# Optimization experiments

Hardware: AMD Instinct MI355X
Metric: run time of the kernel (lower is better)

The kernel has to match this reference:

```python
import jax, jax.numpy as jnp
import numpy as np

VOCAB, EDIM, HDIM, ODIM = 100000, 128, 128, 10
BN_EPS = 1e-3  # keras BatchNormalization default epsilon


def _bn(x, gamma, beta, axes):
    # training-mode batch norm (batch statistics), as in a Keras training step
    m = jnp.mean(x, axis=axes, keepdims=True)
    v = jnp.var(x, axis=axes, keepdims=True)
    return gamma * (x - m) * jax.lax.rsqrt(v + BN_EPS) + beta


def _lstm_last(x, mask, W, U, b):
    # Keras LSTM, gate order [i, f, c, o]; masked steps carry state through.
    # x: [B,T,E], mask: [B,T] bool. Returns final hidden state [B,H].
    B, T, _ = x.shape
    H = U.shape[0]
    xg = jnp.einsum('bte,eg->btg', x, W) + b  # precomputed input projections [B,T,4H]

    def step(carry, inp):
        h, c = carry
        g, m = inp                      # g: [B,4H], m: [B]
        g = g + h @ U
        i, f, cc, o = jnp.split(g, 4, axis=-1)
        c_new = jax.nn.sigmoid(f) * c + jax.nn.sigmoid(i) * jnp.tanh(cc)
        h_new = jax.nn.sigmoid(o) * jnp.tanh(c_new)
        m = m[:, None]
        return (jnp.where(m, h_new, h), jnp.where(m, c_new, c)), None

    init = (jnp.zeros((B, H), x.dtype), jnp.zeros((B, H), x.dtype))
    (h, _), _ = jax.lax.scan(step, init, (xg.transpose(1, 0, 2), mask.T))
    return h


def setup_inputs() -> dict:
    key = jax.random.key(0)
    ks = jax.random.split(key, 12)
    s = 0.05
    ids = jax.random.randint(ks[0], (128, 1024), 0, VOCAB)
    return {
        'ids': ids,
        'embed_table': jax.random.normal(ks[1], (VOCAB, EDIM), jnp.float32) * s,
        'gamma1': jnp.ones((EDIM,), jnp.float32),
        'beta1': jnp.zeros((EDIM,), jnp.float32),
        'Wf': jax.random.normal(ks[2], (EDIM, 4 * HDIM), jnp.float32) * s,
        'Uf': jax.random.normal(ks[3], (HDIM, 4 * HDIM), jnp.float32) * s,
        'bf': jnp.zeros((4 * HDIM,), jnp.float32),
        'Wb': jax.random.normal(ks[4], (EDIM, 4 * HDIM), jnp.float32) * s,
        'Ub': jax.random.normal(ks[5], (HDIM, 4 * HDIM), jnp.float32) * s,
        'bb': jnp.zeros((4 * HDIM,), jnp.float32),
        'gamma2': jnp.ones((2 * HDIM,), jnp.float32),
        'beta2': jnp.zeros((2 * HDIM,), jnp.float32),
        'Wd': jax.random.normal(ks[6], (2 * HDIM, ODIM), jnp.float32) * s,
        'bd': jnp.zeros((ODIM,), jnp.float32),
    }


def reference(ids, embed_table, gamma1, beta1, Wf, Uf, bf, Wb, Ub, bb,
              gamma2, beta2, Wd, bd):
    mask = ids != 0                              # mask_zero=True
    x = embed_table[ids]                         # [B,T,E]
    x = _bn(x, gamma1, beta1, axes=(0, 1))
    h_fwd = _lstm_last(x, mask, Wf, Uf, bf)      # forward direction
    h_bwd = _lstm_last(x[:, ::-1], mask[:, ::-1], Wb, Ub, bb)  # go_backwards
    h = jnp.concatenate([h_fwd, h_bwd], axis=-1)  # merge_mode='concat' -> [B,2H]
    h = _bn(h, gamma2, beta2, axes=(0,))
    return jax.nn.softmax(h @ Wd + bd, axis=-1)
```

## Files before the change

### kernel.cpp

```cpp
#include <hip/hip_runtime.h>
#include <hip/hip_bf16.h>
#include <stdint.h>

#define VOCAB  100000
#define EDIM   128
#define HDIM   128
#define T_LEN  1024
#define BATCH  128
#define GDIM   512
#define NROWS  (BATCH*T_LEN)
#define BN_EPS 1e-3f

using short8 = __attribute__((ext_vector_type(8))) short;
using f32x4  = __attribute__((ext_vector_type(4))) float;

#define WS_SCALE  0u
#define WS_SHIFT  512u
#define WS_PSUM   1024u
#define WS_PSQ    (WS_PSUM + 524288u)
#define WS_HCAT   (WS_PSQ + 524288u)
#define WS_FRAGS  (WS_HCAT + 131072u)
#define WS_XN     (WS_FRAGS + 524288u)

#define SGI_K (-1.4426950408889634f)
#define SGC_K ( 2.8853900817779268f)

__device__ __forceinline__ short f2bf(float f) {
    uint32_t u = __float_as_uint(f);
    return (short)((u + 0x7fffu + ((u >> 16) & 1u)) >> 16);
}

#define BAR() asm volatile("s_waitcnt lgkmcnt(0)\n\ts_barrier" ::: "memory")

__global__ void k_bn1_partial(const int* __restrict__ ids,
                              const float* __restrict__ tab,
                              float* __restrict__ psum, float* __restrict__ psq) {
    __shared__ float ls[256], lq[256];
    int f = threadIdx.x & 127, rr = threadIdx.x >> 7;
    int r0 = blockIdx.x * 128;
    float s = 0.f, q = 0.f;
    for (int r = rr; r < 128; r += 2) {
        int id = ids[r0 + r];
        float v = tab[(size_t)id * EDIM + f];
        s += v; q += v * v;
    }
    ls[threadIdx.x] = s; lq[threadIdx.x] = q;
    __syncthreads();
    if (threadIdx.x < 128) {
        psum[blockIdx.x * 128 + f] = ls[f] + ls[f + 128];
        psq [blockIdx.x * 128 + f] = lq[f] + lq[f + 128];
    }
}

__global__ void k_bn1_final(const float* __restrict__ psum, const float* __restrict__ psq,
                            const float* __restrict__ gamma, const float* __restrict__ beta,
                            float* __restrict__ scale, float* __restrict__ shift) {
    int f = threadIdx.x;
    float s = 0.f, q = 0.f;
    for (int p = 0; p < 1024; ++p) { s += psum[p * 128 + f]; q += psq[p * 128 + f]; }
    const float inv_n = 1.0f / (float)NROWS;
    float m  = s * inv_n;
    float v  = q * inv_n - m * m;
    float sc = gamma[f] * rsqrtf(v + BN_EPS);
    scale[f] = sc;
    shift[f] = beta[f] - m * sc;
}

__global__ void k_packmask(const int* __restrict__ ids, unsigned long long* __restrict__ mwords) {
    int gid = blockIdx.x * 1024 + threadIdx.x;
    unsigned long long bal = __ballot(ids[gid] != 0);
    if ((threadIdx.x & 63) == 0) mwords[gid >> 6] = bal;
}

__global__ void k_embed_norm(const int* __restrict__ ids,
                             const float* __restrict__ tab,
                             const float* __restrict__ scale,
                             const float* __restrict__ shift,
                             short* __restrict__ xn) {
    int gid = blockIdx.x * blockDim.x + threadIdx.x;
    int row = gid >> 4, seg = gid & 15;
    int id  = ids[row];
    const float* src = tab + (size_t)id * EDIM + seg * 8;
    short8 out;
#pragma unroll
    for (int j = 0; j < 8; ++j) {
        float v = scale[seg * 8 + j] * src[j] + shift[seg * 8 + j];
        out[j] = f2bf(v);
    }
    *(short8*)(xn + (size_t)row * EDIM + seg * 8) = out;
}

__global__ void k_prepack(const float* __restrict__ Wf, const float* __restrict__ Uf,
                          const float* __restrict__ Wb, const float* __restrict__ Ub,
                          short* __restrict__ frags) {
    int gid = blockIdx.x * blockDim.x + threadIdx.x;
    int l  = gid & 63;
    int f  = (gid >> 6) & 31;
    int w  = (gid >> 11) & 7;
    int d  = gid >> 14;
    int s    = f >> 4;
    int gate = (f >> 2) & 3;
    int kc   = f & 3;
    const float* M = s ? (d ? Ub : Uf) : (d ? Wb : Wf);
    const float gs = (gate == 2) ? SGC_K : SGI_K;
    int rbase = 32 * kc + 8 * (l >> 4);
    int col   = 128 * gate + 16 * w + (l & 15);
    short8 out;
#pragma unroll
    for (int j = 0; j < 8; ++j) out[j] = f2bf(gs * M[(size_t)(rbase + j) * GDIM + col]);
    *(short8*)(frags + (size_t)gid * 8) = out;
}

#define MFMA(A, B, C) __builtin_amdgcn_mfma_f32_16x16x32_bf16((A), (B), (C), 0, 0, 0)
#define S8(x) __builtin_bit_cast(short8, x)

__global__ void __launch_bounds__(512, 2)
k_lstm(const short* __restrict__ xn,
       const short* __restrict__ frags,
       const unsigned long long* __restrict__ mwords,
       const float* __restrict__ bf_, const float* __restrict__ bb_,
       float* __restrict__ hcat) {
    const int d   = blockIdx.x >> 7;
    const int b   = blockIdx.x & 127;
    const int tid = threadIdx.x;
    const int w   = tid >> 6, l = tid & 63, g = l >> 4, li = l & 15;

    __shared__ float xg_lds[2][16][512];
    __shared__ __align__(16) short h_s[2][HDIM];

    float* const xgf = &xg_lds[0][0][0];
    float* const xgr = xgf + (w * 16 + li) * 4;

    const short8* wsrc = (const short8*)frags + (size_t)(d * 8 + w) * 32 * 64 + l;

    short8 wq00 = wsrc[0*64],  wq01 = wsrc[1*64],  wq02 = wsrc[2*64],  wq03 = wsrc[3*64];
    short8 wq10 = wsrc[4*64],  wq11 = wsrc[5*64],  wq12 = wsrc[6*64],  wq13 = wsrc[7*64];
    short8 wq20 = wsrc[8*64],  wq21 = wsrc[9*64],  wq22 = wsrc[10*64], wq23 = wsrc[11*64];
    short8 wq30 = wsrc[12*64], wq31 = wsrc[13*64], wq32 = wsrc[14*64], wq33 = wsrc[15*64];

    short8 u00 = wsrc[(16+0)*64],  u01 = wsrc[(16+1)*64],  u02 = wsrc[(16+2)*64],  u03 = wsrc[(16+3)*64];
    short8 u10 = wsrc[(16+4)*64],  u11 = wsrc[(16+5)*64],  u12 = wsrc[(16+6)*64],  u13 = wsrc[(16+7)*64];
    short8 u20 = wsrc[(16+8)*64],  u21 = wsrc[(16+9)*64],  u22 = wsrc[(16+10)*64], u23 = wsrc[(16+11)*64];
    short8 u30 = wsrc[(16+12)*64], u31 = wsrc[(16+13)*64], u32 = wsrc[(16+14)*64], u33 = wsrc[(16+15)*64];

    const float* bias = d ? bb_ : bf_;
    const float bia0 = bias[0*128 + w*16 + li] * SGI_K;
    const float bia1 = bias[1*128 + w*16 + li] * SGI_K;
    const float bia2 = bias[2*128 + w*16 + li] * SGC_K;
    const float bia3 = bias[3*128 + w*16 + li] * SGI_K;

    if (tid < HDIM) h_s[0][tid] = 0;
    float c_reg = 0.f, h_reg = 0.f;

    const f32x4 Z = {0.f, 0.f, 0.f, 0.f};

    uint4 ga0, ga1, ga2, ga3;
#define GATHER(C_) { \
        int s0_ = 16 * (C_) + li; \
        int p_  = d ? (T_LEN - 1 - s0_) : s0_; \
        const uint4* gb_ = (const uint4*)xn + (size_t)(b * T_LEN + p_) * 16; \
        ga0 = gb_[g]; ga1 = gb_[4 + g]; ga2 = gb_[8 + g]; ga3 = gb_[12 + g]; \
    }

#define XWGATE(GG, W0, W1, W2, W3, BIA, BUF) { \
        f32x4 ax = {(BIA), (BIA), (BIA), (BIA)}; \
        ax = MFMA(S8(ga0), W0, ax); \
        ax = MFMA(S8(ga1), W1, ax); \
        ax = MFMA(S8(ga2), W2, ax); \
        ax = MFMA(S8(ga3), W3, ax); \
        float* dst_ = xgf + (BUF) * 8192 + (w * 16 + li) * 4 + (GG); \
        dst_[(4*g+0)*512] = ax[0]; dst_[(4*g+1)*512] = ax[1]; \
        dst_[(4*g+2)*512] = ax[2]; dst_[(4*g+3)*512] = ax[3]; \
    }

    GATHER(0);
    XWGATE(0, wq00, wq01, wq02, wq03, bia0, 0);
    XWGATE(1, wq10, wq11, wq12, wq13, bia1, 0);
    XWGATE(2, wq20, wq21, wq22, wq23, bia2, 0);
    XWGATE(3, wq30, wq31, wq32, wq33, bia3, 0);
    __syncthreads();

    float xa0, xa1, xa2, xa3, xb0, xb1, xb2, xb3;
    {
        const f32x4 xv0 = *(const f32x4*)(xgr);
        xa0 = xv0[0]; xa1 = xv0[1]; xa2 = xv0[2]; xa3 = xv0[3];
    }

#define STEP(J, XC0, XC1, XC2, XC3, XN0, XN1, XN2, XN3) { \
        const uint4* hp_ = (const uint4*)(h_s[(J) & 1]); \
        uint4 hf0 = hp_[g], hf1 = hp_[4 + g], hf2 = hp_[8 + g], hf3 = hp_[12 + g]; \
        if (c < 63) { \
            if ((J) == 8)  XWGATE(0, wq00, wq01, wq02, wq03, bia0, ((c + 1) & 1)); \
            if ((J) == 9)  XWGATE(1, wq10, wq11, wq12, wq13, bia1, ((c + 1) & 1)); \
            if ((J) == 10) XWGATE(2, wq20, wq21, wq22, wq23, bia2, ((c + 1) & 1)); \
            if ((J) == 11) XWGATE(3, wq30, wq31, wq32, wq33, bia3, ((c + 1) & 1)); \
        } \
        f32x4 p0 = MFMA(S8(hf0), u00, Z); \
        f32x4 p1 = MFMA(S8(hf0), u10, Z); \
        f32x4 p2 = MFMA(S8(hf0), u20, Z); \
        f32x4 p3 = MFMA(S8(hf0), u30, Z); \
        f32x4 q0 = MFMA(S8(hf2), u02, Z); \
        f32x4 q1 = MFMA(S8(hf2), u12, Z); \
        f32x4 q2 = MFMA(S8(hf2), u22, Z); \
        f32x4 q3 = MFMA(S8(hf2), u32, Z); \
        p0 = MFMA(S8(hf1), u01, p0); \
        p1 = MFMA(S8(hf1), u11, p1); \
        p2 = MFMA(S8(hf1), u21, p2); \
        p3 = MFMA(S8(hf1), u31, p3); \
        q0 = MFMA(S8(hf3), u03, q0); \
        q1 = MFMA(S8(hf3), u13, q1); \
        q2 = MFMA(S8(hf3), u23, q2); \
        q3 = MFMA(S8(hf3), u33, q3); \
        if (!((c == 63) && ((J) == 15))) { \
            const f32x4 xv_ = *(const f32x4*)(xgr + (((J) < 15) ? (c & 1) : ((c + 1) & 1)) * 8192 \
                                                  + (((J) + 1) & 15) * 512); \
            XN0 = xv_[0]; XN1 = xv_[1]; XN2 = xv_[2]; XN3 = xv_[3]; \
        } \
        { \
            float gi = (XC0) + (p0[0] + q0[0]); \
            float gf = (XC1) + (p1[0] + q1[0]); \
            float gc = (XC2) + (p2[0] + q2[0]); \
            float go = (XC3) + (p3[0] + q3[0]); \
            float si = __builtin_amdgcn_rcpf(1.f + exp2f(gi)); \
            float sf = __builtin_amdgcn_rcpf(1.f + exp2f(gf)); \
            float so = __builtin_amdgcn_rcpf(1.f + exp2f(go)); \
            float tc = __builtin_fmaf(-2.f, __builtin_amdgcn_rcpf(1.f + exp2f(gc)), 1.f); \
            float cn = __builtin_fmaf(sf, c_reg, si * tc); \
            float th = __builtin_fmaf(-2.f, __builtin_amdgcn_rcpf(1.f + exp2f(cn * SGC_K)), 1.f); \
            float hn = so * th; \
            if (mb & (1u << (J))) { c_reg = cn; h_reg = hn; } \
            uint32_t pk_; \
            asm("v_cvt_pk_bf16_f32 %0, %1, %2" : "=v"(pk_) : "v"(h_reg), "v"(h_reg)); \
            if (l < 16) h_s[((J) + 1) & 1][w * 16 + li] = (short)pk_; \
        } \
        BAR(); \
    }

#pragma unroll 1
    for (int c = 0; c < 64; ++c) {
        if (c < 63) GATHER(c + 1);
        int cc_ = d ? 63 - c : c;
        unsigned long long mw_ = mwords[(size_t)b * 16 + (cc_ >> 2)];
        uint32_t mb = (uint32_t)(mw_ >> ((cc_ & 3) * 16)) & 0xFFFFu;
        if (d) mb = __builtin_bitreverse32(mb) >> 16;
        STEP(0,  xa0, xa1, xa2, xa3, xb0, xb1, xb2, xb3)
        STEP(1,  xb0, xb1, xb2, xb3, xa0, xa1, xa2, xa3)
        STEP(2,  xa0, xa1, xa2, xa3, xb0, xb1, xb2, xb3)
        STEP(3,  xb0, xb1, xb2, xb3, xa0, xa1, xa2, xa3)
        STEP(4,  xa0, xa1, xa2, xa3, xb0, xb1, xb2, xb3)
        STEP(5,  xb0, xb1, xb2, xb3, xa0, xa1, xa2, xa3)
        STEP(6,  xa0, xa1, xa2, xa3, xb0, xb1, xb2, xb3)
        STEP(7,  xb0, xb1, xb2, xb3, xa0, xa1, xa2, xa3)
        STEP(8,  xa0, xa1, xa2, xa3, xb0, xb1, xb2, xb3)
        STEP(9,  xb0, xb1, xb2, xb3, xa0, xa1, xa2, xa3)
        STEP(10, xa0, xa1, xa2, xa3, xb0, xb1, xb2, xb3)
        STEP(11, xb0, xb1, xb2, xb3, xa0, xa1, xa2, xa3)
        STEP(12, xa0, xa1, xa2, xa3, xb0, xb1, xb2, xb3)
        STEP(13, xb0, xb1, xb2, xb3, xa0, xa1, xa2, xa3)
        STEP(14, xa0, xa1, xa2, xa3, xb0, xb1, xb2, xb3)
        STEP(15, xb0, xb1, xb2, xb3, xa0, xa1, xa2, xa3)
    }

    if (l < 16) hcat[b * 256 + d * 128 + w * 16 + li] = h_reg;
}

__global__ void k_head(const float* __restrict__ hcat,
                       const float* __restrict__ gamma2, const float* __restrict__ beta2,
                       const float* __restrict__ Wd, const float* __restrict__ bd,
                       float* __restrict__ out) {
    __shared__ float sc_s[256], sh_s[256];
    __shared__ float logits[BATCH * 10];
    int tid = threadIdx.x;
    if (tid < 256) {
        float s = 0.f, q = 0.f;
        for (int bb = 0; bb < BATCH; ++bb) { float v = hcat[bb * 256 + tid]; s += v; q += v * v; }
        float m  = s / (float)BATCH;
        float v  = q / (float)BATCH - m * m;
        float sc = gamma2[tid] * rsqrtf(v + BN_EPS);
        sc_s[tid] = sc;
        sh_s[tid] = beta2[tid] - m * sc;
    }
    __syncthreads();
    {
        int bb = tid >> 3, oq = tid & 7;
        float acc0 = bd[oq], acc1 = (oq < 2) ? bd[8 + oq] : 0.f;
        for (int k = 0; k < 256; ++k) {
            float hv = sc_s[k] * hcat[bb * 256 + k] + sh_s[k];
            acc0 += hv * Wd[k * 10 + oq];
            if (oq < 2) acc1 += hv * Wd[k * 10 + 8 + oq];
        }
        logits[bb * 10 + oq] = acc0;
        if (oq < 2) logits[bb * 10 + 8 + oq] = acc1;
    }
    __syncthreads();
    if (tid < BATCH) {
        float lm = -1e30f;
#pragma unroll
        for (int o = 0; o < 10; ++o) lm = fmaxf(lm, logits[tid * 10 + o]);
        float e[10], s = 0.f;
#pragma unroll
        for (int o = 0; o < 10; ++o) { e[o] = __expf(logits[tid * 10 + o] - lm); s += e[o]; }
        float inv = __builtin_amdgcn_rcpf(s);
#pragma unroll
        for (int o = 0; o < 10; ++o) out[tid * 10 + o] = e[o] * inv;
    }
}

extern "C" void kernel_launch(void* const* d_in, const int* in_sizes, int n_in,
                              void* d_out, int out_size, void* d_ws, size_t ws_size,
                              hipStream_t stream) {
    const int*   ids = (const int*)  d_in[0];
    const float* tab = (const float*)d_in[1];
    const float* g1  = (const float*)d_in[2];
    const float* b1  = (const float*)d_in[3];
    const float* Wf  = (const float*)d_in[4];
    const float* Uf  = (const float*)d_in[5];
    const float* bfv = (const float*)d_in[6];
    const float* Wb  = (const float*)d_in[7];
    const float* Ub  = (const float*)d_in[8];
    const float* bbv = (const float*)d_in[9];
    const float* g2  = (const float*)d_in[10];
    const float* b2  = (const float*)d_in[11];
    const float* Wd  = (const float*)d_in[12];
    const float* bd  = (const float*)d_in[13];

    char*  ws    = (char*)d_ws;
    float* scale = (float*)(ws + WS_SCALE);
    float* shift = (float*)(ws + WS_SHIFT);
    float* psum  = (float*)(ws + WS_PSUM);
    float* psq   = (float*)(ws + WS_PSQ);
    float* hcat  = (float*)(ws + WS_HCAT);
    short* fragp = (short*)(ws + WS_FRAGS);
    short* xnp   = (short*)(ws + WS_XN);
    unsigned long long* mwords = (unsigned long long*)(ws + WS_PSUM);

    k_bn1_partial<<<1024, 256, 0, stream>>>(ids, tab, psum, psq);
    k_bn1_final  <<<1, 128, 0, stream>>>(psum, psq, g1, b1, scale, shift);
    k_packmask   <<<128, 1024, 0, stream>>>(ids, mwords);
    k_embed_norm <<<8192, 256, 0, stream>>>(ids, tab, scale, shift, xnp);
    k_prepack    <<<128, 256, 0, stream>>>(Wf, Uf, Wb, Ub, fragp);
    k_lstm       <<<256, 512, 0, stream>>>(xnp, fragp, mwords, bfv, bbv, hcat);
    k_head       <<<1, 1024, 0, stream>>>(hcat, g2, b2, Wd, bd, (float*)d_out);
}
```

Baseline: 645.2 us.

## Halve LSTM block to four waves, each computing two hidden slices

The recurrent LSTM kernel now runs 256 threads per block instead of 512. Each wave computes two 16-column hidden slices, holding two sets of recurrent-weight fragments in registers. Input-projection weights are now reloaded from global memory each time they are used rather than kept in registers. The aim is to cut the cost of the per-step block barrier and LDS traffic by using fewer waves. In exchange, each wave runs twice as many dependent MFMAs and twice the gate math per timestep on the serial recurrence path, and the prologue does a redundant extra projection pass.

```diff
diff --git a/kernel.cpp b/kernel.cpp
--- a/kernel.cpp
+++ b/kernel.cpp
@@ -114,7 +114,7 @@
 #define MFMA(A, B, C) __builtin_amdgcn_mfma_f32_16x16x32_bf16((A), (B), (C), 0, 0, 0)
 #define S8(x) __builtin_bit_cast(short8, x)
 
-__global__ void __launch_bounds__(512, 2)
+__global__ void __launch_bounds__(256, 1)
 k_lstm(const short* __restrict__ xn,
        const short* __restrict__ frags,
        const unsigned long long* __restrict__ mwords,
@@ -129,30 +129,38 @@
     __shared__ __align__(16) short h_s[2][HDIM];
 
     float* const xgf = &xg_lds[0][0][0];
-    float* const xgr = xgf + (w * 16 + li) * 4;
-
-    const short8* wsrc = (const short8*)frags + (size_t)(d * 8 + w) * 32 * 64 + l;
-
-    short8 wq00 = wsrc[0*64],  wq01 = wsrc[1*64],  wq02 = wsrc[2*64],  wq03 = wsrc[3*64];
-    short8 wq10 = wsrc[4*64],  wq11 = wsrc[5*64],  wq12 = wsrc[6*64],  wq13 = wsrc[7*64];
-    short8 wq20 = wsrc[8*64],  wq21 = wsrc[9*64],  wq22 = wsrc[10*64], wq23 = wsrc[11*64];
-    short8 wq30 = wsrc[12*64], wq31 = wsrc[13*64], wq32 = wsrc[14*64], wq33 = wsrc[15*64];
-
-    short8 u00 = wsrc[(16+0)*64],  u01 = wsrc[(16+1)*64],  u02 = wsrc[(16+2)*64],  u03 = wsrc[(16+3)*64];
-    short8 u10 = wsrc[(16+4)*64],  u11 = wsrc[(16+5)*64],  u12 = wsrc[(16+6)*64],  u13 = wsrc[(16+7)*64];
-    short8 u20 = wsrc[(16+8)*64],  u21 = wsrc[(16+9)*64],  u22 = wsrc[(16+10)*64], u23 = wsrc[(16+11)*64];
-    short8 u30 = wsrc[(16+12)*64], u31 = wsrc[(16+13)*64], u32 = wsrc[(16+14)*64], u33 = wsrc[(16+15)*64];
+
+    const short8* wsA = (const short8*)frags + (size_t)(d * 8 + 2 * w) * 2048 + l;
+    const short8* wsB = wsA + 2048;
+
+    short8 uA00 = wsA[(16+0)*64],  uA01 = wsA[(16+1)*64],  uA02 = wsA[(16+2)*64],  uA03 = wsA[(16+3)*64];
+    short8 uA10 = wsA[(16+4)*64],  uA11 = wsA[(16+5)*64],  uA12 = wsA[(16+6)*64],  uA13 = wsA[(16+7)*64];
+    short8 uA20 = wsA[(16+8)*64],  uA21 = wsA[(16+9)*64],  uA22 = wsA[(16+10)*64], uA23 = wsA[(16+11)*64];
+    short8 uA30 = wsA[(16+12)*64], uA31 = wsA[(16+13)*64], uA32 = wsA[(16+14)*64], uA33 = wsA[(16+15)*64];
+    short8 uB00 = wsB[(16+0)*64],  uB01 = wsB[(16+1)*64],  uB02 = wsB[(16+2)*64],  uB03 = wsB[(16+3)*64];
+    short8 uB10 = wsB[(16+4)*64],  uB11 = wsB[(16+5)*64],  uB12 = wsB[(16+6)*64],  uB13 = wsB[(16+7)*64];
+    short8 uB20 = wsB[(16+8)*64],  uB21 = wsB[(16+9)*64],  uB22 = wsB[(16+10)*64], uB23 = wsB[(16+11)*64];
+    short8 uB30 = wsB[(16+12)*64], uB31 = wsB[(16+13)*64], uB32 = wsB[(16+14)*64], uB33 = wsB[(16+15)*64];
 
     const float* bias = d ? bb_ : bf_;
-    const float bia0 = bias[0*128 + w*16 + li] * SGI_K;
-    const float bia1 = bias[1*128 + w*16 + li] * SGI_K;
-    const float bia2 = bias[2*128 + w*16 + li] * SGC_K;
-    const float bia3 = bias[3*128 + w*16 + li] * SGI_K;
+    const float biaA0 = bias[0*128 + 32*w + li]      * SGI_K;
+    const float biaA1 = bias[1*128 + 32*w + li]      * SGI_K;
+    const float biaA2 = bias[2*128 + 32*w + li]      * SGC_K;
+    const float biaA3 = bias[3*128 + 32*w + li]      * SGI_K;
+    const float biaB0 = bias[0*128 + 32*w + 16 + li] * SGI_K;
+    const float biaB1 = bias[1*128 + 32*w + 16 + li] * SGI_K;
+    const float biaB2 = bias[2*128 + 32*w + 16 + li] * SGC_K;
+    const float biaB3 = bias[3*128 + 32*w + 16 + li] * SGI_K;
 
     if (tid < HDIM) h_s[0][tid] = 0;
-    float c_reg = 0.f, h_reg = 0.f;
+    float c_regA = 0.f, h_regA = 0.f, c_regB = 0.f, h_regB = 0.f;
 
     const f32x4 Z = {0.f, 0.f, 0.f, 0.f};
+
+    float* rdA_c = xgf + (32 * w + li) * 4;
+    float* rdA_n = rdA_c + 8192;
+    float* rdB_c = rdA_c + 64;
+    float* rdB_n = rdB_c + 8192;
 
     uint4 ga0, ga1, ga2, ga3;
 #define GATHER(C_) { \
@@ -162,76 +170,103 @@
         ga0 = gb_[g]; ga1 = gb_[4 + g]; ga2 = gb_[8 + g]; ga3 = gb_[12 + g]; \
     }
 
-#define XWGATE(GG, W0, W1, W2, W3, BIA, BUF) { \
-        f32x4 ax = {(BIA), (BIA), (BIA), (BIA)}; \
-        ax = MFMA(S8(ga0), W0, ax); \
-        ax = MFMA(S8(ga1), W1, ax); \
-        ax = MFMA(S8(ga2), W2, ax); \
-        ax = MFMA(S8(ga3), W3, ax); \
-        float* dst_ = xgf + (BUF) * 8192 + (w * 16 + li) * 4 + (GG); \
-        dst_[(4*g+0)*512] = ax[0]; dst_[(4*g+1)*512] = ax[1]; \
-        dst_[(4*g+2)*512] = ax[2]; dst_[(4*g+3)*512] = ax[3]; \
+#define XWT(G_, S_, BIA_, DSTBASE_) { \
+        const short8* wp_ = (S_) ? wsB : wsA; \
+        short8 w0_ = wp_[((G_)*4+0)*64], w1_ = wp_[((G_)*4+1)*64]; \
+        short8 w2_ = wp_[((G_)*4+2)*64], w3_ = wp_[((G_)*4+3)*64]; \
+        f32x4 ax = {(BIA_), (BIA_), (BIA_), (BIA_)}; \
+        ax = MFMA(S8(ga0), w0_, ax); \
+        ax = MFMA(S8(ga1), w1_, ax); \
+        ax = MFMA(S8(ga2), w2_, ax); \
+        ax = MFMA(S8(ga3), w3_, ax); \
+        float* wd_ = (DSTBASE_) + (S_) * 64 + (G_); \
+        wd_[(4*g+0)*512] = ax[0]; wd_[(4*g+1)*512] = ax[1]; \
+        wd_[(4*g+2)*512] = ax[2]; wd_[(4*g+3)*512] = ax[3]; \
     }
 
     GATHER(0);
-    XWGATE(0, wq00, wq01, wq02, wq03, bia0, 0);
-    XWGATE(1, wq10, wq11, wq12, wq13, bia1, 0);
-    XWGATE(2, wq20, wq21, wq22, wq23, bia2, 0);
-    XWGATE(3, wq30, wq31, wq32, wq33, bia3, 0);
-    __syncthreads();
-
-    float xa0, xa1, xa2, xa3, xb0, xb1, xb2, xb3;
-    {
-        const f32x4 xv0 = *(const f32x4*)(xgr);
-        xa0 = xv0[0]; xa1 = xv0[1]; xa2 = xv0[2]; xa3 = xv0[3];
-    }
-
-#define STEP(J, XC0, XC1, XC2, XC3, XN0, XN1, XN2, XN3) { \
+    XWT(0,0,biaA0, rdA_c - (32*w+li)*4)
+    XWT(0,1,biaB0, rdA_c - (32*w+li)*4)
+    XWT(1,0,biaA1, rdA_c - (32*w+li)*4)
+    XWT(1,1,biaB1, rdA_c - (32*w+li)*4)
+    XWT(2,0,biaA2, rdA_c - (32*w+li)*4)
+    XWT(2,1,biaB2, rdA_c - (32*w+li)*4)
+    XWT(3,0,biaA3, rdA_c - (32*w+li)*4)
+    XWT(3,1,biaB3, rdA_c - (32*w+li)*4)
+    __syncthreads();
+
+    GATHER(0);
+    XWT(0,0,biaA0, rdA_c)
+    XWT(0,1,biaB0, rdA_c)
+    XWT(1,0,biaA1, rdA_c)
+    XWT(1,1,biaB1, rdA_c)
+    XWT(2,0,biaA2, rdA_c)
+    XWT(2,1,biaB2, rdA_c)
+    XWT(3,0,biaA3, rdA_c)
+    XWT(3,1,biaB3, rdA_c)
+    __syncthreads();
+
+    f32x4 xva = *(const f32x4*)rdA_c;
+    f32x4 xvb = *(const f32x4*)rdB_c;
+    f32x4 yva, yvb;
+
+#define XWBIA(J) ((J)==8?biaA0:(J)==9?biaB0:(J)==10?biaA1:(J)==11?biaB1: \
+                  (J)==12?biaA2:(J)==13?biaB2:(J)==14?biaA3:biaB3)
+
+#define STEP(J, CVA, CVB, NVA, NVB) { \
         const uint4* hp_ = (const uint4*)(h_s[(J) & 1]); \
         uint4 hf0 = hp_[g], hf1 = hp_[4 + g], hf2 = hp_[8 + g], hf3 = hp_[12 + g]; \
-        if (c < 63) { \
-            if ((J) == 8)  XWGATE(0, wq00, wq01, wq02, wq03, bia0, ((c + 1) & 1)); \
-            if ((J) == 9)  XWGATE(1, wq10, wq11, wq12, wq13, bia1, ((c + 1) & 1)); \
-            if ((J) == 10) XWGATE(2, wq20, wq21, wq22, wq23, bia2, ((c + 1) & 1)); \
-            if ((J) == 11) XWGATE(3, wq30, wq31, wq32, wq33, bia3, ((c + 1) & 1)); \
+        if (!((c == 63) && ((J) == 15))) { \
+            const float* ra_ = ((J) < 15) ? rdA_c : rdA_n; \
+            const float* rb_ = ((J) < 15) ? rdB_c : rdB_n; \
+            NVA = *(const f32x4*)(ra_ + (((J) + 1) & 15) * 512); \
+            NVB = *(const f32x4*)(rb_ + (((J) + 1) & 15) * 512); \
         } \
-        f32x4 p0 = MFMA(S8(hf0), u00, Z); \
-        f32x4 p1 = MFMA(S8(hf0), u10, Z); \
-        f32x4 p2 = MFMA(S8(hf0), u20, Z); \
-        f32x4 p3 = MFMA(S8(hf0), u30, Z); \
-        f32x4 q0 = MFMA(S8(hf2), u02, Z); \
-        f32x4 q1 = MFMA(S8(hf2), u12, Z); \
-        f32x4 q2 = MFMA(S8(hf2), u22, Z); \
-        f32x4 q3 = MFMA(S8(hf2), u32, Z); \
-        p0 = MFMA(S8(hf1), u01, p0); \
-        p1 = MFMA(S8(hf1), u11, p1); \
-        p2 = MFMA(S8(hf1), u21, p2); \
-        p3 = MFMA(S8(hf1), u31, p3); \
-        q0 = MFMA(S8(hf3), u03, q0); \
-        q1 = MFMA(S8(hf3), u13, q1); \
-        q2 = MFMA(S8(hf3), u23, q2); \
-        q3 = MFMA(S8(hf3), u33, q3); \
-        if (!((c == 63) && ((J) == 15))) { \
-            const f32x4 xv_ = *(const f32x4*)(xgr + (((J) < 15) ? (c & 1) : ((c + 1) & 1)) * 8192 \
-                                                  + (((J) + 1) & 15) * 512); \
-            XN0 = xv_[0]; XN1 = xv_[1]; XN2 = xv_[2]; XN3 = xv_[3]; \
+        f32x4 pA0, pA1, pA2, pA3, pB0, pB1, pB2, pB3; \
+        pA0 = MFMA(S8(hf0), uA00, Z);  pB0 = MFMA(S8(hf0), uB00, Z); \
+        pA1 = MFMA(S8(hf0), uA10, Z);  pB1 = MFMA(S8(hf0), uB10, Z); \
+        pA2 = MFMA(S8(hf0), uA20, Z);  pB2 = MFMA(S8(hf0), uB20, Z); \
+        pA3 = MFMA(S8(hf0), uA30, Z);  pB3 = MFMA(S8(hf0), uB30, Z); \
+        pA0 = MFMA(S8(hf1), uA01, pA0); pB0 = MFMA(S8(hf1), uB01, pB0); \
+        pA1 = MFMA(S8(hf1), uA11, pA1); pB1 = MFMA(S8(hf1), uB11, pB1); \
+        pA2 = MFMA(S8(hf1), uA21, pA2); pB2 = MFMA(S8(hf1), uB21, pB2); \
+        pA3 = MFMA(S8(hf1), uA31, pA3); pB3 = MFMA(S8(hf1), uB31, pB3); \
+        pA0 = MFMA(S8(hf2), uA02, pA0); pB0 = MFMA(S8(hf2), uB02, pB0); \
+        pA1 = MFMA(S8(hf2), uA12, pA1); pB1 = MFMA(S8(hf2), uB12, pB1); \
+        pA2 = MFMA(S8(hf2), uA22, pA2); pB2 = MFMA(S8(hf2), uB22, pB2); \
+        pA3 = MFMA(S8(hf2), uA32, pA3); pB3 = MFMA(S8(hf2), uB32, pB3); \
+        pA0 = MFMA(S8(hf3), uA03, pA0); pB0 = MFMA(S8(hf3), uB03, pB0); \
+        pA1 = MFMA(S8(hf3), uA13, pA1); pB1 = MFMA(S8(hf3), uB13, pB1); \
+        pA2 = MFMA(S8(hf3), uA23, pA2); pB2 = MFMA(S8(hf3), uB23, pB2); \
+        pA3 = MFMA(S8(hf3), uA33, pA3); pB3 = MFMA(S8(hf3), uB33, pB3); \
+        if (((J) >= 8) && (c < 63)) { \
+            XWT(((J)-8)>>1, (J)&1, XWBIA(J), rdA_n) \
         } \
         { \
-            float gi = (XC0) + (p0[0] + q0[0]); \
-            float gf = (XC1) + (p1[0] + q1[0]); \
-            float gc = (XC2) + (p2[0] + q2[0]); \
-            float go = (XC3) + (p3[0] + q3[0]); \
-            float si = __builtin_amdgcn_rcpf(1.f + exp2f(gi)); \
-            float sf = __builtin_amdgcn_rcpf(1.f + exp2f(gf)); \
-            float so = __builtin_amdgcn_rcpf(1.f + exp2f(go)); \
-            float tc = __builtin_fmaf(-2.f, __builtin_amdgcn_rcpf(1.f + exp2f(gc)), 1.f); \
-            float cn = __builtin_fmaf(sf, c_reg, si * tc); \
-            float th = __builtin_fmaf(-2.f, __builtin_amdgcn_rcpf(1.f + exp2f(cn * SGC_K)), 1.f); \
-            float hn = so * th; \
-            if (mb & (1u << (J))) { c_reg = cn; h_reg = hn; } \
+            float giA = CVA[0] + pA0[0], gfA = CVA[1] + pA1[0]; \
+            float gcA = CVA[2] + pA2[0], goA = CVA[3] + pA3[0]; \
+            float giB = CVB[0] + pB0[0], gfB = CVB[1] + pB1[0]; \
+            float gcB = CVB[2] + pB2[0], goB = CVB[3] + pB3[0]; \
+            float siA = __builtin_amdgcn_rcpf(1.f + exp2f(giA)); \
+            float sfA = __builtin_amdgcn_rcpf(1.f + exp2f(gfA)); \
+            float soA = __builtin_amdgcn_rcpf(1.f + exp2f(goA)); \
+            float tcA = __builtin_fmaf(-2.f, __builtin_amdgcn_rcpf(1.f + exp2f(gcA)), 1.f); \
+            float siB = __builtin_amdgcn_rcpf(1.f + exp2f(giB)); \
+            float sfB = __builtin_amdgcn_rcpf(1.f + exp2f(gfB)); \
+            float soB = __builtin_amdgcn_rcpf(1.f + exp2f(goB)); \
+            float tcB = __builtin_fmaf(-2.f, __builtin_amdgcn_rcpf(1.f + exp2f(gcB)), 1.f); \
+            float cnA = __builtin_fmaf(sfA, c_regA, siA * tcA); \
+            float cnB = __builtin_fmaf(sfB, c_regB, siB * tcB); \
+            float thA = __builtin_fmaf(-2.f, __builtin_amdgcn_rcpf(1.f + exp2f(cnA * SGC_K)), 1.f); \
+            float thB = __builtin_fmaf(-2.f, __builtin_amdgcn_rcpf(1.f + exp2f(cnB * SGC_K)), 1.f); \
+            float hnA = soA * thA, hnB = soB * thB; \
+            if (mb & (1u << (J))) { c_regA = cnA; h_regA = hnA; c_regB = cnB; h_regB = hnB; } \
             uint32_t pk_; \
-            asm("v_cvt_pk_bf16_f32 %0, %1, %2" : "=v"(pk_) : "v"(h_reg), "v"(h_reg)); \
-            if (l < 16) h_s[((J) + 1) & 1][w * 16 + li] = (short)pk_; \
+            asm("v_cvt_pk_bf16_f32 %0, %1, %2" : "=v"(pk_) : "v"(h_regA), "v"(h_regB)); \
+            if (l < 16) { \
+                h_s[((J) + 1) & 1][32 * w + li]      = (short)pk_; \
+                h_s[((J) + 1) & 1][32 * w + 16 + li] = (short)(pk_ >> 16); \
+            } \
         } \
         BAR(); \
     }
@@ -243,25 +278,31 @@
         unsigned long long mw_ = mwords[(size_t)b * 16 + (cc_ >> 2)];
         uint32_t mb = (uint32_t)(mw_ >> ((cc_ & 3) * 16)) & 0xFFFFu;
         if (d) mb = __builtin_bitreverse32(mb) >> 16;
-        STEP(0,  xa0, xa1, xa2, xa3, xb0, xb1, xb2, xb3)
-        STEP(1,  xb0, xb1, xb2, xb3, xa0, xa1, xa2, xa3)
-        STEP(2,  xa0, xa1, xa2, xa3, xb0, xb1, xb2, xb3)
-        STEP(3,  xb0, xb1, xb2, xb3, xa0, xa1, xa2, xa3)
-        STEP(4,  xa0, xa1, xa2, xa3, xb0, xb1, xb2, xb3)
-        STEP(5,  xb0, xb1, xb2, xb3, xa0, xa1, xa2, xa3)
-        STEP(6,  xa0, xa1, xa2, xa3, xb0, xb1, xb2, xb3)
-        STEP(7,  xb0, xb1, xb2, xb3, xa0, xa1, xa2, xa3)
-        STEP(8,  xa0, xa1, xa2, xa3, xb0, xb1, xb2, xb3)
-        STEP(9,  xb0, xb1, xb2, xb3, xa0, xa1, xa2, xa3)
-        STEP(10, xa0, xa1, xa2, xa3, xb0, xb1, xb2, xb3)
-        STEP(11, xb0, xb1, xb2, xb3, xa0, xa1, xa2, xa3)
-        STEP(12, xa0, xa1, xa2, xa3, xb0, xb1, xb2, xb3)
-        STEP(13, xb0, xb1, xb2, xb3, xa0, xa1, xa2, xa3)
-        STEP(14, xa0, xa1, xa2, xa3, xb0, xb1, xb2, xb3)
-        STEP(15, xb0, xb1, xb2, xb3, xa0, xa1, xa2, xa3)
-    }
-
-    if (l < 16) hcat[b * 256 + d * 128 + w * 16 + li] = h_reg;
+        STEP(0,  xva, xvb, yva, yvb)
+        STEP(1,  yva, yvb, xva, xvb)
+        STEP(2,  xva, xvb, yva, yvb)
+        STEP(3,  yva, yvb, xva, xvb)
+        STEP(4,  xva, xvb, yva, yvb)
+        STEP(5,  yva, yvb, xva, xvb)
+        STEP(6,  xva, xvb, yva, yvb)
+        STEP(7,  yva, yvb, xva, xvb)
+        STEP(8,  xva, xvb, yva, yvb)
+        STEP(9,  yva, yvb, xva, xvb)
+        STEP(10, xva, xvb, yva, yvb)
+        STEP(11, yva, yvb, xva, xvb)
+        STEP(12, xva, xvb, yva, yvb)
+        STEP(13, yva, yvb, xva, xvb)
+        STEP(14, xva, xvb, yva, yvb)
+        STEP(15, yva, yvb, xva, xvb)
+        { float* t_;
+          t_ = rdA_c; rdA_c = rdA_n; rdA_n = t_;
+          t_ = rdB_c; rdB_c = rdB_n; rdB_n = t_; }
+    }
+
+    if (l < 16) {
+        hcat[b * 256 + d * 128 + 32 * w + li]      = h_regA;
+        hcat[b * 256 + d * 128 + 32 * w + 16 + li] = h_regB;
+    }
 }
 
 __global__ void k_head(const float* __restrict__ hcat,
@@ -339,6 +380,6 @@
     k_packmask   <<<128, 1024, 0, stream>>>(ids, mwords);
     k_embed_norm <<<8192, 256, 0, stream>>>(ids, tab, scale, shift, xnp);
     k_prepack    <<<128, 256, 0, stream>>>(Wf, Uf, Wb, Ub, fragp);
-    k_lstm       <<<256, 512, 0, stream>>>(xnp, fragp, mwords, bfv, bbv, hcat);
+    k_lstm       <<<256, 256, 0, stream>>>(xnp, fragp, mwords, bfv, bbv, hcat);
     k_head       <<<1, 1024, 0, stream>>>(hcat, g2, b2, Wd, bd, (float*)d_out);
 }
```

Result: slower. 846.9 us (+31.3%).
